# Kernel tuning notes

Measured on AMD Instinct MI355X. Metric: run time of the kernel, lower is better.

Reference implementation:

```python
import jax, jax.numpy as jnp
import numpy as np

CLASS_NUM = 31
KERNEL_NUM = 5
KERNEL_MUL = 2.0


def setup_inputs() -> dict:
    key = jax.random.key(0)
    k1, k2, k3, k4 = jax.random.split(key, 4)
    B, D = 4096, 256
    source = jax.random.normal(k1, (B, D), dtype=jnp.float32)
    target = jax.random.normal(k2, (B, D), dtype=jnp.float32)
    s_label = jax.random.randint(k3, (B,), 0, CLASS_NUM, dtype=jnp.int64)
    t_label = jax.random.uniform(k4, (B, CLASS_NUM), dtype=jnp.float32)
    return {"source": source, "target": target, "s_label": s_label, "t_label": t_label}


def _cal_weight(s_label, t_label):
    # Source: one-hot, column-normalized (empty classes -> divide by 100)
    s_onehot = jax.nn.one_hot(s_label, CLASS_NUM, dtype=jnp.float32)
    s_cnt = jnp.sum(s_onehot, axis=0)
    s_vec = s_onehot / jnp.where(s_cnt == 0, 100.0, s_cnt)
    # Target: soft probs, column-normalized (detached in original)
    t_prob = jax.lax.stop_gradient(t_label)
    t_cnt = jnp.sum(t_prob, axis=0)
    t_vec = t_prob / jnp.where(t_cnt == 0, 100.0, t_cnt)
    # Classes present in BOTH source labels and target argmax predictions
    t_arg = jnp.argmax(t_prob, axis=1)
    t_present = jnp.sum(jax.nn.one_hot(t_arg, CLASS_NUM, dtype=jnp.float32), axis=0) > 0
    mask = ((s_cnt > 0) & t_present).astype(jnp.float32)
    n_idx = jnp.maximum(jnp.sum(mask), 1.0)
    s_vec = s_vec * mask
    t_vec = t_vec * mask
    w_ss = (s_vec @ s_vec.T) / n_idx
    w_tt = (t_vec @ t_vec.T) / n_idx
    w_st = (s_vec @ t_vec.T) / n_idx
    return w_ss, w_tt, w_st


def reference(source, target, s_label, t_label):
    B = source.shape[0]
    w_ss, w_tt, w_st = _cal_weight(s_label, t_label)

    # Multi-bandwidth RBF kernel over concatenated samples
    total = jnp.concatenate([source, target], axis=0)  # [2B, D]
    sq = jnp.sum(total * total, axis=1)
    l2 = jnp.maximum(sq[:, None] + sq[None, :] - 2.0 * (total @ total.T), 0.0)  # [2B, 2B]

    n = 2 * B
    bw = jnp.sum(jax.lax.stop_gradient(l2)) / float(max(n * n - n, 1))
    bw = jnp.maximum(bw, 1e-6) / (KERNEL_MUL ** (KERNEL_NUM // 2))
    kernels = jnp.zeros_like(l2)
    for i in range(KERNEL_NUM):
        kernels = kernels + jnp.exp(-l2 / jnp.maximum(bw * KERNEL_MUL ** i, 1e-6))

    ss = kernels[:B, :B]
    tt = kernels[B:, B:]
    st = kernels[:B, B:]
    loss = jnp.sum(w_ss * ss + w_tt * tt - 2.0 * w_st * st)
    return loss
```

## Files before the change

### kernel.cpp

```cpp
#include <hip/hip_runtime.h>


#define B 4096
#define D 256
#define C 31
#define N2 8192
#define NTILE 64
#define NBLK (NTILE * (NTILE + 1) / 2)

typedef __attribute__((ext_vector_type(8))) short bf16x8;
typedef __attribute__((ext_vector_type(4))) float f32x4;

struct WS {
  double sum_sq;
  double Msum[256];
  int s_cnt[32];
  float t_cnt[32];
  int t_pres[32];
  float s_div[32], t_div[32];
  float inv_n_idx;
  float inv_d4;
  float sq[N2];
  int slab[N2];
  float sdv[N2];
  alignas(16) unsigned char Thi8[(size_t)N2 * D];
  alignas(16) unsigned short vhi[(size_t)N2 * 32];
  alignas(16) float v[(size_t)N2 * 32];
  alignas(16) double part[NBLK];
};

static __device__ __forceinline__ unsigned short f2bf(float f) {
  unsigned int u = __float_as_uint(f);
  return (unsigned short)((u + 0x7fffu + ((u >> 16) & 1u)) >> 16);
}
static __device__ __forceinline__ float bf2f(unsigned short s) {
  return __uint_as_float(((unsigned int)s) << 16);
}

#define GLD16(gsrc, ldst)                                                     \
  __builtin_amdgcn_global_load_lds(                                           \
      (const __attribute__((address_space(1))) void*)(gsrc),                  \
      (__attribute__((address_space(3))) void*)(ldst), 16, 0, 0)

__global__ void k0_init(WS* __restrict__ ws) {
  int tid = threadIdx.x;
  if (tid == 0) ws->sum_sq = 0.0;
  if (tid < 32) {
    ws->s_cnt[tid] = 0;
    ws->t_cnt[tid] = 0.f;
    ws->t_pres[tid] = 0;
  }
  ws->Msum[tid] = 0.0;
}

__global__ void kA1_stats(const int* __restrict__ s_label,
                          const float* __restrict__ t_label,
                          WS* __restrict__ ws) {
  __shared__ int ls[32];
  __shared__ float lt[32];
  __shared__ int lpres[32];
  int tid = threadIdx.x, lane = tid & 63;
  if (tid < 32) { ls[tid] = 0; lt[tid] = 0.f; lpres[tid] = 0; }
  __syncthreads();
  int row = blockIdx.x * 256 + tid;
  atomicAdd(&ls[s_label[row]], 1);
  const float* r = t_label + (size_t)row * C;
  float best = -1e30f;
  int barg = 0;
#pragma unroll
  for (int c = 0; c < C; ++c) {
    float x = r[c];
    if (x > best) { best = x; barg = c; }
    float s = x;
#pragma unroll
    for (int off = 32; off; off >>= 1) s += __shfl_down(s, off, 64);
    if (lane == 0) atomicAdd(&lt[c], s);
  }
  lpres[barg] = 1;
  __syncthreads();
  if (tid < 32) {
    if (ls[tid]) atomicAdd(&ws->s_cnt[tid], ls[tid]);
    atomicAdd(&ws->t_cnt[tid], lt[tid]);
    if (lpres[tid]) ws->t_pres[tid] = 1;
  }
}

__global__ void kA2_final(WS* __restrict__ ws) {
  int tid = threadIdx.x;
  int m = 0;
  if (tid < 32) {
    int cnt = ws->s_cnt[tid];
    m = (tid < C) && (cnt > 0) && (ws->t_pres[tid] != 0);
    ws->s_div[tid] = m ? 1.f / (float)cnt : 0.f;
    float t = ws->t_cnt[tid];
    float ta = (t == 0.f) ? 100.f : t;
    ws->t_div[tid] = m ? 1.f / ta : 0.f;
  }
  unsigned long long bal = __ballot(m);
  if (tid == 0) ws->inv_n_idx = 1.f / fmaxf((float)__popcll(bal), 1.f);
}

__global__ __launch_bounds__(256) void kB_prep(const float* __restrict__ src,
                                               const float* __restrict__ tgt,
                                               const int* __restrict__ s_label,
                                               const float* __restrict__ t_label,
                                               WS* __restrict__ ws) {
  int tid = threadIdx.x, w = tid >> 6, lane = tid & 63;
  int r0 = blockIdx.x * 32;
  __shared__ float rsq[32];
  __shared__ float colp[4][256];
  float ca0 = 0.f, ca1 = 0.f, ca2 = 0.f, ca3 = 0.f;
  int sc = lane >> 4, gl = (lane >> 1) & 7, hf = lane & 1;
#pragma unroll
  for (int i = 0; i < 8; ++i) {
    int rr = w * 8 + i;
    int p = r0 + rr;
    const float* rp = (p < B) ? src + (size_t)p * D : tgt + (size_t)(p - B) * D;
    float4 x = *(const float4*)(rp + lane * 4);
    unsigned int pk = __builtin_amdgcn_cvt_pk_fp8_f32(x.x, x.y, 0, false);
    pk = __builtin_amdgcn_cvt_pk_fp8_f32(x.z, x.w, pk, true);
    int gp = (gl + p + (p >> 1)) & 7;
    *(unsigned int*)(&ws->Thi8[(size_t)p * D + sc * 64 + gp * 8 + hf * 4]) = pk;
    ca0 += x.x; ca1 += x.y; ca2 += x.z; ca3 += x.w;
    float s = x.x * x.x + x.y * x.y + x.z * x.z + x.w * x.w;
#pragma unroll
    for (int off = 32; off; off >>= 1) s += __shfl_down(s, off, 64);
    if (lane == 0) rsq[rr] = s;
  }
  colp[w][lane * 4 + 0] = ca0;
  colp[w][lane * 4 + 1] = ca1;
  colp[w][lane * 4 + 2] = ca2;
  colp[w][lane * 4 + 3] = ca3;
  __syncthreads();
  if (tid < 32) {
    int p = r0 + tid;
    ws->sq[p] = rsq[tid];
    if (p < B) {
      int lb = s_label[p];
      ws->slab[p] = lb;
      ws->sdv[p] = ws->s_div[lb];
    } else {
      ws->slab[p] = 0;
      ws->sdv[p] = 0.f;
    }
  }
  if (tid < 64) {
    float ss = (tid < 32) ? rsq[tid] : 0.f;
#pragma unroll
    for (int off = 32; off; off >>= 1) ss += __shfl_down(ss, off, 64);
    if (tid == 0) atomicAdd(&ws->sum_sq, (double)ss);
  }
  atomicAdd(&ws->Msum[tid],
            (double)(colp[0][tid] + colp[1][tid] + colp[2][tid] + colp[3][tid]));
  int vr = tid >> 3, cb = (tid & 7) * 4;
  int p = r0 + vr;
  float vals[4];
#pragma unroll
  for (int j = 0; j < 4; ++j) {
    int c = cb + j;
    float val = 0.f;
    if (c < C) {
      if (p < B)
        val = (s_label[p] == c) ? ws->s_div[c] : 0.f;
      else
        val = -t_label[(size_t)(p - B) * C + c] * ws->t_div[c];
    }
    vals[j] = val;
  }
  float4 vf; vf.x = vals[0]; vf.y = vals[1]; vf.z = vals[2]; vf.w = vals[3];
  *(float4*)(&ws->v[(size_t)p * 32 + cb]) = vf;
  ushort4 vh;
  vh.x = f2bf(vals[0]); vh.y = f2bf(vals[1]);
  vh.z = f2bf(vals[2]); vh.w = f2bf(vals[3]);
  *(ushort4*)(&ws->vhi[(size_t)p * 32 + cb]) = vh;
}

__global__ void kC_bw(WS* __restrict__ ws) {
  int lane = threadIdx.x;
  double msq = 0.0;
#pragma unroll
  for (int i = 0; i < 4; ++i) {
    double m = ws->Msum[i * 64 + lane];
    msq += m * m;
  }
#pragma unroll
  for (int off = 32; off; off >>= 1) msq += __shfl_down(msq, off, 64);
  if (lane == 0) {
    double S = ws->sum_sq;
    double n = (double)N2;
    double sum_l2 = 2.0 * n * S - 2.0 * msq;
    double bw = sum_l2 / (n * n - n);
    bw = fmax(bw, 1e-6) * 0.25;
    double dc4 = fmax(bw * 16.0, 1e-6);
    ws->inv_d4 = (float)(1.0 / dc4);
  }
}

template <int KIND, bool DIAG>
static __device__ __forceinline__ float epi_ss_st(
    const f32x4 (&acc)[4][4], const WS* __restrict__ ws,
    const unsigned short* Vsw, int p0, int q0, int wr, int wc, int mrow,
    int quad) {
  float cinv = ws->inv_d4;
  float k2 = 2.f * cinv;
  float cq[4], sdq[4];
  int lq[4];
#pragma unroll
  for (int tj = 0; tj < 4; ++tj) {
    int q = q0 + wc + tj * 16 + mrow;
    cq[tj] = -cinv * ws->sq[q];
    if (KIND == 0) {
      lq[tj] = ws->slab[q];
      sdq[tj] = ws->sdv[q];
    }
  }
  float local = 0.f;
#pragma unroll
  for (int ti = 0; ti < 4; ++ti) {
#pragma unroll
    for (int rg = 0; rg < 4; ++rg) {
      int p = p0 + wr + ti * 16 + quad * 4 + rg;
      float cpl = -cinv * ws->sq[p];
      int lp = ws->slab[p];
      float sp = ws->sdv[p];
#pragma unroll
      for (int tj = 0; tj < 4; ++tj) {
        float z = fminf(fmaf(k2, acc[ti][tj][rg], cpl + cq[tj]), 0.f);
        float y = __expf(z);
        float kv = y;
        y *= y; kv += y;
        y *= y; kv += y;
        y *= y; kv += y;
        y *= y; kv += y;
        float wv;
        if (KIND == 0) {
          wv = (lp == lq[tj]) ? sp * sdq[tj] : 0.f;
        } else {
          int ql = wc + tj * 16 + mrow;
          wv = sp * bf2f(Vsw[ql * 32 + ((lp + ql) & 31)]);
        }
        if (DIAG) {
          int q = q0 + wc + tj * 16 + mrow;
          float f = (q > p) ? 2.f : ((q == p) ? 1.f : 0.f);
          local = fmaf(wv * f, kv, local);
        } else {
          local = fmaf(wv, kv, local);
        }
      }
    }
  }
  if (!DIAG) local *= 2.f;
  return local;
}

template <bool DIAG>
static __device__ __forceinline__ float epi_tt(const f32x4 (&acc)[4][4],
                                               const WS* __restrict__ ws,
                                               const unsigned short* SA,
                                               const unsigned short* SB,
                                               int p0, int q0, int wr, int wc,
                                               int mrow, int quad) {
  float cinv = ws->inv_d4;
  float k2 = 2.f * cinv;
  float cq[4];
#pragma unroll
  for (int tj = 0; tj < 4; ++tj)
    cq[tj] = -cinv * ws->sq[q0 + wc + tj * 16 + mrow];
  float cp[16];
#pragma unroll
  for (int ti = 0; ti < 4; ++ti)
#pragma unroll
    for (int rg = 0; rg < 4; ++rg)
      cp[ti * 4 + rg] = -cinv * ws->sq[p0 + wr + ti * 16 + quad * 4 + rg];
  bf16x8 af[4], bfr[4];
#pragma unroll
  for (int ti = 0; ti < 4; ++ti)
    af[ti] = *(const bf16x8*)(SA + (wr + ti * 16 + mrow) * 32 + quad * 8);
#pragma unroll
  for (int tj = 0; tj < 4; ++tj)
    bfr[tj] = *(const bf16x8*)(SB + (wc + tj * 16 + mrow) * 32 + quad * 8);
  float local = 0.f;
#pragma unroll
  for (int ti = 0; ti < 4; ++ti) {
#pragma unroll
    for (int tj = 0; tj < 4; ++tj) {
      f32x4 wv4 = __builtin_amdgcn_mfma_f32_16x16x32_bf16(
          af[ti], bfr[tj], (f32x4){0.f, 0.f, 0.f, 0.f}, 0, 0, 0);
#pragma unroll
      for (int rg = 0; rg < 4; ++rg) {
        float z = fminf(fmaf(k2, acc[ti][tj][rg], cp[ti * 4 + rg] + cq[tj]), 0.f);
        float y = __expf(z);
        float kv = y;
        y *= y; kv += y;
        y *= y; kv += y;
        y *= y; kv += y;
        y *= y; kv += y;
        if (DIAG) {
          int p = p0 + wr + ti * 16 + quad * 4 + rg;
          int q = q0 + wc + tj * 16 + mrow;
          float f = (q > p) ? 2.f : ((q == p) ? 1.f : 0.f);
          local = fmaf(wv4[rg] * f, kv, local);
        } else {
          local = fmaf(wv4[rg], kv, local);
        }
      }
    }
  }
  if (!DIAG) local *= 2.f;
  return local;
}

__global__ __launch_bounds__(256, 3) void k3_main(WS* __restrict__ ws) {
  int tid = threadIdx.x, w = tid >> 6, lane = tid & 63;
  int lin0 = blockIdx.x;
  int e = (lin0 & 7) * (NBLK / 8) + (lin0 >> 3);
  int b = 0, nb = 484, rem = e;
  while (rem >= nb) { rem -= nb; ++b; nb -= 64; }
  int base = b * 8;
  int bq_, r;
  if (rem < 36) {
    bq_ = 0;
    while ((bq_ + 1) * (bq_ + 2) / 2 <= rem) ++bq_;
    r = rem - (bq_ * (bq_ + 1)) / 2;
  } else {
    int t = rem - 36;
    bq_ = 8 + (t >> 3);
    r = t & 7;
  }
  int bp = base + r, bq = base + bq_;
  int p0 = bp * 128, q0 = bq * 128;

  bool is_ss = (bq < 32);
  bool is_tt = (bp >= 32);

  __shared__ __align__(16) unsigned char S[2][2][8192];
  unsigned short* Vsw = (unsigned short*)&S[0][0][0];
  unsigned short* SA = (unsigned short*)&S[0][0][0];
  unsigned short* SB = (unsigned short*)&S[0][1][0];
  double* red = (double*)&S[1][0][0];

  const int wr = (w >> 1) * 64, wc = (w & 1) * 64;
  const int mrow = lane & 15, quad = lane >> 4;
  f32x4 acc[4][4];
#pragma unroll
  for (int i = 0; i < 4; ++i)
#pragma unroll
    for (int j = 0; j < 4; ++j) acc[i][j] = (f32x4){0.f, 0.f, 0.f, 0.f};

  const unsigned char* T8 = ws->Thi8;
  int rA = tid >> 2, cb16 = (tid & 3) * 16, cp8 = (tid & 3) * 8;
  const unsigned char* a_lo = T8 + (size_t)(p0 + rA) * D + cb16;
  const unsigned char* a_hi = a_lo + (size_t)64 * D;
  const unsigned char* b_lo = T8 + (size_t)(q0 + rA) * D + cb16;
  const unsigned char* b_hi = b_lo + (size_t)64 * D;

#define STAGE(bufi, off)                                                      \
  do {                                                                        \
    GLD16(a_lo + (off), &S[bufi][0][w * 1024]);                               \
    GLD16(a_hi + (off), &S[bufi][0][w * 1024 + 4096]);                        \
    GLD16(b_lo + (off), &S[bufi][1][w * 1024]);                               \
    GLD16(b_hi + (off), &S[bufi][1][w * 1024 + 4096]);                        \
  } while (0)

  int aAdr[4], bAdr[4];
#pragma unroll
  for (int ti = 0; ti < 4; ++ti) {
    int Ra = wr + ti * 16 + mrow;
    aAdr[ti] = Ra * 64 + (((quad + Ra + (Ra >> 1)) & 7) << 3);
    int Rb = wc + ti * 16 + mrow;
    bAdr[ti] = Rb * 64 + (((quad + Rb + (Rb >> 1)) & 7) << 3);
  }

  STAGE(0, 0);
  __syncthreads();

#pragma unroll
  for (int i = 0; i < 4; ++i) {
    const int bufi = i & 1;
    if (i < 3) STAGE(bufi ^ 1, (i + 1) * 64);
    if (i == 3 && is_tt) {
      const unsigned short* gA = ws->vhi + (size_t)(p0 + rA) * 32 + cp8;
      const unsigned short* gB = ws->vhi + (size_t)(q0 + rA) * 32 + cp8;
      GLD16(gA, &S[0][0][w * 1024]);
      GLD16(gA + (size_t)64 * 32, &S[0][0][w * 1024 + 4096]);
      GLD16(gB, &S[0][1][w * 1024]);
      GLD16(gB + (size_t)64 * 32, &S[0][1][w * 1024 + 4096]);
    }
    const unsigned char* fb = &S[bufi][0][0];
#pragma unroll
    for (int t = 0; t < 2; ++t) {
      const int x = t << 5;
      long aF[4], bF[4];
#pragma unroll
      for (int ti = 0; ti < 4; ++ti)
        aF[ti] = *(const long*)(fb + (aAdr[ti] ^ x));
#pragma unroll
      for (int tj = 0; tj < 4; ++tj)
        bF[tj] = *(const long*)(fb + 8192 + (bAdr[tj] ^ x));
#pragma unroll
      for (int ti = 0; ti < 4; ++ti)
#pragma unroll
        for (int tj = 0; tj < 4; ++tj)
          acc[ti][tj] = __builtin_amdgcn_mfma_f32_16x16x32_fp8_fp8(
              aF[ti], bF[tj], acc[ti][tj], 0, 0, 0);
    }
    if (i < 3) __syncthreads();
  }

  if (!is_ss && !is_tt) {
    int rr = tid >> 1, h = (tid & 1) * 16;
    const float* vrow = ws->v + (size_t)(q0 + rr) * 32 + h;
#pragma unroll
    for (int j = 0; j < 16; ++j)
      Vsw[rr * 32 + ((h + j + rr) & 31)] = f2bf(vrow[j]);
  }
  __syncthreads();

  float local;
  if (is_ss) {
    if (bp == bq)
      local = epi_ss_st<0, true>(acc, ws, Vsw, p0, q0, wr, wc, mrow, quad);
    else
      local = epi_ss_st<0, false>(acc, ws, Vsw, p0, q0, wr, wc, mrow, quad);
  } else if (!is_tt) {
    local = epi_ss_st<1, false>(acc, ws, Vsw, p0, q0, wr, wc, mrow, quad);
  } else {
    if (bp == bq)
      local = epi_tt<true>(acc, ws, SA, SB, p0, q0, wr, wc, mrow, quad);
    else
      local = epi_tt<false>(acc, ws, SA, SB, p0, q0, wr, wc, mrow, quad);
  }

  double dl = (double)local;
#pragma unroll
  for (int off = 32; off; off >>= 1) dl += __shfl_down(dl, off, 64);
  if (lane == 0) red[w] = dl;
  __syncthreads();
  if (tid == 0) ws->part[lin0] = red[0] + red[1] + red[2] + red[3];
#undef STAGE
}

__global__ __launch_bounds__(256) void k4_out(WS* __restrict__ ws,
                                              float* __restrict__ out) {
  __shared__ double sh[4];
  int tid = threadIdx.x, w = tid >> 6, lane = tid & 63;
  double s = 0.0;
  for (int i = tid; i < NBLK; i += 256) s += ws->part[i];
#pragma unroll
  for (int off = 32; off; off >>= 1) s += __shfl_down(s, off, 64);
  if (lane == 0) sh[w] = s;
  __syncthreads();
  if (tid == 0)
    out[0] = (float)((sh[0] + sh[1] + sh[2] + sh[3]) * (double)ws->inv_n_idx);
}

extern "C" void kernel_launch(void* const* d_in, const int* in_sizes, int n_in,
                              void* d_out, int out_size, void* d_ws, size_t ws_size,
                              hipStream_t stream) {
  const float* src = (const float*)d_in[0];
  const float* tgt = (const float*)d_in[1];
  const int* s_label = (const int*)d_in[2];
  const float* t_label = (const float*)d_in[3];
  float* out = (float*)d_out;
  WS* ws = (WS*)d_ws;

  k0_init<<<1, 256, 0, stream>>>(ws);
  kA1_stats<<<16, 256, 0, stream>>>(s_label, t_label, ws);
  kA2_final<<<1, 64, 0, stream>>>(ws);
  kB_prep<<<256, 256, 0, stream>>>(src, tgt, s_label, t_label, ws);
  kC_bw<<<1, 64, 0, stream>>>(ws);
  k3_main<<<NBLK, 256, 0, stream>>>(ws);
  k4_out<<<1, 256, 0, stream>>>(ws, out);
}
```

Baseline: 132.5 us.

## Fuse prep stages into fewer launches and stage per-tile row data in LDS

Folds the label statistics into the feature prep kernel, and merges the bandwidth computation, weight finalisation and v-vector build into one kernel. This cuts the pre-pass from four launches to two. The main kernel now loads each tile's squared norms, labels and per-row divisors into LDS once, and prefetches the bf16 v rows during the MMA loop instead of converting fp32 rows after it. In exchange the per-class stats use more shared atomics per row, and the v build becomes a separate 32-block pass.

```diff
diff --git a/kernel.cpp b/kernel.cpp
--- a/kernel.cpp
+++ b/kernel.cpp
@@ -1,4 +1,5 @@
 #include <hip/hip_runtime.h>
+#include <cstddef>
 
 
 #define B 4096
@@ -17,7 +18,6 @@
   int s_cnt[32];
   float t_cnt[32];
   int t_pres[32];
-  float s_div[32], t_div[32];
   float inv_n_idx;
   float inv_d4;
   float sq[N2];
@@ -53,62 +53,19 @@
   ws->Msum[tid] = 0.0;
 }
 
-__global__ void kA1_stats(const int* __restrict__ s_label,
-                          const float* __restrict__ t_label,
-                          WS* __restrict__ ws) {
-  __shared__ int ls[32];
-  __shared__ float lt[32];
-  __shared__ int lpres[32];
-  int tid = threadIdx.x, lane = tid & 63;
-  if (tid < 32) { ls[tid] = 0; lt[tid] = 0.f; lpres[tid] = 0; }
-  __syncthreads();
-  int row = blockIdx.x * 256 + tid;
-  atomicAdd(&ls[s_label[row]], 1);
-  const float* r = t_label + (size_t)row * C;
-  float best = -1e30f;
-  int barg = 0;
-#pragma unroll
-  for (int c = 0; c < C; ++c) {
-    float x = r[c];
-    if (x > best) { best = x; barg = c; }
-    float s = x;
-#pragma unroll
-    for (int off = 32; off; off >>= 1) s += __shfl_down(s, off, 64);
-    if (lane == 0) atomicAdd(&lt[c], s);
-  }
-  lpres[barg] = 1;
-  __syncthreads();
-  if (tid < 32) {
-    if (ls[tid]) atomicAdd(&ws->s_cnt[tid], ls[tid]);
-    atomicAdd(&ws->t_cnt[tid], lt[tid]);
-    if (lpres[tid]) ws->t_pres[tid] = 1;
-  }
-}
-
-__global__ void kA2_final(WS* __restrict__ ws) {
-  int tid = threadIdx.x;
-  int m = 0;
-  if (tid < 32) {
-    int cnt = ws->s_cnt[tid];
-    m = (tid < C) && (cnt > 0) && (ws->t_pres[tid] != 0);
-    ws->s_div[tid] = m ? 1.f / (float)cnt : 0.f;
-    float t = ws->t_cnt[tid];
-    float ta = (t == 0.f) ? 100.f : t;
-    ws->t_div[tid] = m ? 1.f / ta : 0.f;
-  }
-  unsigned long long bal = __ballot(m);
-  if (tid == 0) ws->inv_n_idx = 1.f / fmaxf((float)__popcll(bal), 1.f);
-}
-
-__global__ __launch_bounds__(256) void kB_prep(const float* __restrict__ src,
-                                               const float* __restrict__ tgt,
-                                               const int* __restrict__ s_label,
-                                               const float* __restrict__ t_label,
-                                               WS* __restrict__ ws) {
+__global__ __launch_bounds__(256) void kPrep(const float* __restrict__ src,
+                                             const float* __restrict__ tgt,
+                                             const int* __restrict__ s_label,
+                                             const float* __restrict__ t_label,
+                                             WS* __restrict__ ws) {
   int tid = threadIdx.x, w = tid >> 6, lane = tid & 63;
   int r0 = blockIdx.x * 32;
   __shared__ float rsq[32];
   __shared__ float colp[4][256];
+  __shared__ int ls[32];
+  __shared__ float lt[32];
+  __shared__ int lpres[32];
+  if (tid < 32) { ls[tid] = 0; lt[tid] = 0.f; lpres[tid] = 0; }
   float ca0 = 0.f, ca1 = 0.f, ca2 = 0.f, ca3 = 0.f;
   int sc = lane >> 4, gl = (lane >> 1) & 7, hf = lane & 1;
 #pragma unroll
@@ -138,10 +95,19 @@
     if (p < B) {
       int lb = s_label[p];
       ws->slab[p] = lb;
-      ws->sdv[p] = ws->s_div[lb];
+      atomicAdd(&ls[lb], 1);
     } else {
       ws->slab[p] = 0;
-      ws->sdv[p] = 0.f;
+      const float* r = t_label + (size_t)(p - B) * C;
+      float best = -1e30f;
+      int barg = 0;
+#pragma unroll
+      for (int c = 0; c < C; ++c) {
+        float x = r[c];
+        if (x > best) { best = x; barg = c; }
+        atomicAdd(&lt[c], x);
+      }
+      lpres[barg] = 1;
     }
   }
   if (tid < 64) {
@@ -152,66 +118,95 @@
   }
   atomicAdd(&ws->Msum[tid],
             (double)(colp[0][tid] + colp[1][tid] + colp[2][tid] + colp[3][tid]));
-  int vr = tid >> 3, cb = (tid & 7) * 4;
-  int p = r0 + vr;
-  float vals[4];
-#pragma unroll
-  for (int j = 0; j < 4; ++j) {
-    int c = cb + j;
-    float val = 0.f;
-    if (c < C) {
-      if (p < B)
-        val = (s_label[p] == c) ? ws->s_div[c] : 0.f;
-      else
-        val = -t_label[(size_t)(p - B) * C + c] * ws->t_div[c];
-    }
-    vals[j] = val;
-  }
-  float4 vf; vf.x = vals[0]; vf.y = vals[1]; vf.z = vals[2]; vf.w = vals[3];
-  *(float4*)(&ws->v[(size_t)p * 32 + cb]) = vf;
-  ushort4 vh;
-  vh.x = f2bf(vals[0]); vh.y = f2bf(vals[1]);
-  vh.z = f2bf(vals[2]); vh.w = f2bf(vals[3]);
-  *(ushort4*)(&ws->vhi[(size_t)p * 32 + cb]) = vh;
-}
-
-__global__ void kC_bw(WS* __restrict__ ws) {
-  int lane = threadIdx.x;
-  double msq = 0.0;
-#pragma unroll
-  for (int i = 0; i < 4; ++i) {
-    double m = ws->Msum[i * 64 + lane];
-    msq += m * m;
-  }
-#pragma unroll
-  for (int off = 32; off; off >>= 1) msq += __shfl_down(msq, off, 64);
-  if (lane == 0) {
-    double S = ws->sum_sq;
-    double n = (double)N2;
-    double sum_l2 = 2.0 * n * S - 2.0 * msq;
-    double bw = sum_l2 / (n * n - n);
-    bw = fmax(bw, 1e-6) * 0.25;
-    double dc4 = fmax(bw * 16.0, 1e-6);
-    ws->inv_d4 = (float)(1.0 / dc4);
+  __syncthreads();
+  if (tid < 32) {
+    if (r0 < B) {
+      if (ls[tid]) atomicAdd(&ws->s_cnt[tid], ls[tid]);
+    } else {
+      atomicAdd(&ws->t_cnt[tid], lt[tid]);
+      if (lpres[tid]) ws->t_pres[tid] = 1;
+    }
+  }
+}
+
+__global__ __launch_bounds__(256) void kFin(const int* __restrict__ s_label,
+                                            const float* __restrict__ t_label,
+                                            WS* __restrict__ ws) {
+  int tid = threadIdx.x;
+  __shared__ float sdiv[32], tdiv[32];
+  if (tid < 64) {
+    int m = 0;
+    if (tid < 32) {
+      int cnt = ws->s_cnt[tid];
+      m = (tid < C) && (cnt > 0) && (ws->t_pres[tid] != 0);
+      sdiv[tid] = m ? 1.f / (float)cnt : 0.f;
+      float t = ws->t_cnt[tid];
+      tdiv[tid] = m ? 1.f / ((t == 0.f) ? 100.f : t) : 0.f;
+    }
+    unsigned long long bal = __ballot(m);
+    if (tid == 0 && blockIdx.x == 0)
+      ws->inv_n_idx = 1.f / fmaxf((float)__popcll(bal), 1.f);
+  } else if (tid < 128 && blockIdx.x == 0) {
+    int lane = tid - 64;
+    double msq = 0.0;
+#pragma unroll
+    for (int i = 0; i < 4; ++i) {
+      double mm = ws->Msum[i * 64 + lane];
+      msq += mm * mm;
+    }
+#pragma unroll
+    for (int off = 32; off; off >>= 1) msq += __shfl_down(msq, off, 64);
+    if (lane == 0) {
+      double S = ws->sum_sq;
+      double n = (double)N2;
+      double sum_l2 = 2.0 * n * S - 2.0 * msq;
+      double bw = sum_l2 / (n * n - n);
+      bw = fmax(bw, 1e-6) * 0.25;
+      ws->inv_d4 = (float)(1.0 / fmax(bw * 16.0, 1e-6));
+    }
+  }
+  __syncthreads();
+  int p = blockIdx.x * 256 + tid;
+  float vrow[32];
+  if (p < B) {
+    int lb = s_label[p];
+    float sv = sdiv[lb];
+    ws->sdv[p] = sv;
+#pragma unroll
+    for (int c = 0; c < 32; ++c) vrow[c] = (c == lb) ? sv : 0.f;
+  } else {
+    ws->sdv[p] = 0.f;
+    const float* r = t_label + (size_t)(p - B) * C;
+#pragma unroll
+    for (int c = 0; c < 32; ++c) vrow[c] = (c < C) ? -r[c] * tdiv[c] : 0.f;
+  }
+#pragma unroll
+  for (int k = 0; k < 8; ++k) {
+    float4 vf;
+    vf.x = vrow[k * 4 + 0]; vf.y = vrow[k * 4 + 1];
+    vf.z = vrow[k * 4 + 2]; vf.w = vrow[k * 4 + 3];
+    *(float4*)(&ws->v[(size_t)p * 32 + k * 4]) = vf;
+    ushort4 vh;
+    vh.x = f2bf(vf.x); vh.y = f2bf(vf.y); vh.z = f2bf(vf.z); vh.w = f2bf(vf.w);
+    *(ushort4*)(&ws->vhi[(size_t)p * 32 + k * 4]) = vh;
   }
 }
 
 template <int KIND, bool DIAG>
 static __device__ __forceinline__ float epi_ss_st(
-    const f32x4 (&acc)[4][4], const WS* __restrict__ ws,
-    const unsigned short* Vsw, int p0, int q0, int wr, int wc, int mrow,
-    int quad) {
-  float cinv = ws->inv_d4;
+    const f32x4 (&acc)[4][4], float cinv, const float* tSq, const int* tSlab,
+    const float* tSdv, const unsigned short* Vsw, int p0, int q0, int wr,
+    int wc, int mrow, int quad) {
   float k2 = 2.f * cinv;
   float cq[4], sdq[4];
   int lq[4];
 #pragma unroll
   for (int tj = 0; tj < 4; ++tj) {
-    int q = q0 + wc + tj * 16 + mrow;
-    cq[tj] = -cinv * ws->sq[q];
+    int iq = 128 + wc + tj * 16 + mrow;
+    cq[tj] = -cinv * tSq[iq];
     if (KIND == 0) {
-      lq[tj] = ws->slab[q];
-      sdq[tj] = ws->sdv[q];
+      lq[tj] = tSlab[iq];
+      sdq[tj] = tSdv[iq];
     }
   }
   float local = 0.f;
@@ -219,10 +214,10 @@
   for (int ti = 0; ti < 4; ++ti) {
 #pragma unroll
     for (int rg = 0; rg < 4; ++rg) {
-      int p = p0 + wr + ti * 16 + quad * 4 + rg;
-      float cpl = -cinv * ws->sq[p];
-      int lp = ws->slab[p];
-      float sp = ws->sdv[p];
+      int ip = wr + ti * 16 + quad * 4 + rg;
+      float cpl = -cinv * tSq[ip];
+      int lp = tSlab[ip];
+      float sp = tSdv[ip];
 #pragma unroll
       for (int tj = 0; tj < 4; ++tj) {
         float z = fminf(fmaf(k2, acc[ti][tj][rg], cpl + cq[tj]), 0.f);
@@ -240,6 +235,7 @@
           wv = sp * bf2f(Vsw[ql * 32 + ((lp + ql) & 31)]);
         }
         if (DIAG) {
+          int p = p0 + ip;
           int q = q0 + wc + tj * 16 + mrow;
           float f = (q > p) ? 2.f : ((q == p) ? 1.f : 0.f);
           local = fmaf(wv * f, kv, local);
@@ -255,23 +251,22 @@
 
 template <bool DIAG>
 static __device__ __forceinline__ float epi_tt(const f32x4 (&acc)[4][4],
-                                               const WS* __restrict__ ws,
+                                               float cinv, const float* tSq,
                                                const unsigned short* SA,
                                                const unsigned short* SB,
                                                int p0, int q0, int wr, int wc,
                                                int mrow, int quad) {
-  float cinv = ws->inv_d4;
   float k2 = 2.f * cinv;
   float cq[4];
 #pragma unroll
   for (int tj = 0; tj < 4; ++tj)
-    cq[tj] = -cinv * ws->sq[q0 + wc + tj * 16 + mrow];
+    cq[tj] = -cinv * tSq[128 + wc + tj * 16 + mrow];
   float cp[16];
 #pragma unroll
   for (int ti = 0; ti < 4; ++ti)
 #pragma unroll
     for (int rg = 0; rg < 4; ++rg)
-      cp[ti * 4 + rg] = -cinv * ws->sq[p0 + wr + ti * 16 + quad * 4 + rg];
+      cp[ti * 4 + rg] = -cinv * tSq[wr + ti * 16 + quad * 4 + rg];
   bf16x8 af[4], bfr[4];
 #pragma unroll
   for (int ti = 0; ti < 4; ++ti)
@@ -332,8 +327,12 @@
 
   bool is_ss = (bq < 32);
   bool is_tt = (bp >= 32);
+  bool is_st = !is_ss && !is_tt;
 
   __shared__ __align__(16) unsigned char S[2][2][8192];
+  __shared__ __align__(16) float tSq[256];
+  __shared__ __align__(16) int tSlab[256];
+  __shared__ __align__(16) float tSdv[256];
   unsigned short* Vsw = (unsigned short*)&S[0][0][0];
   unsigned short* SA = (unsigned short*)&S[0][0][0];
   unsigned short* SB = (unsigned short*)&S[0][1][0];
@@ -371,6 +370,8 @@
     bAdr[ti] = Rb * 64 + (((quad + Rb + (Rb >> 1)) & 7) << 3);
   }
 
+  uint4 stv0 = {0, 0, 0, 0}, stv1 = {0, 0, 0, 0};
+
   STAGE(0, 0);
   __syncthreads();
 
@@ -378,6 +379,22 @@
   for (int i = 0; i < 4; ++i) {
     const int bufi = i & 1;
     if (i < 3) STAGE(bufi ^ 1, (i + 1) * 64);
+    if (i == 0 && w == 0) {
+      int l32 = lane & 31;
+      const float* s1 = ((lane < 32) ? ws->sq + p0 : ws->sq + q0) + l32 * 4;
+      GLD16(s1, tSq);
+      const int* s2 = ((lane < 32) ? ws->slab + p0 : ws->slab + q0) + l32 * 4;
+      GLD16(s2, tSlab);
+      const float* s3 = ((lane < 32) ? ws->sdv + p0 : ws->sdv + q0) + l32 * 4;
+      GLD16(s3, tSdv);
+    }
+    if (i == 2 && is_st) {
+      const uint4* vsrc = (const uint4*)(ws->vhi +
+                                         (size_t)(q0 + (tid >> 1)) * 32 +
+                                         (tid & 1) * 16);
+      stv0 = vsrc[0];
+      stv1 = vsrc[1];
+    }
     if (i == 3 && is_tt) {
       const unsigned short* gA = ws->vhi + (size_t)(p0 + rA) * 32 + cp8;
       const unsigned short* gB = ws->vhi + (size_t)(q0 + rA) * 32 + cp8;
@@ -407,28 +424,35 @@
     if (i < 3) __syncthreads();
   }
 
-  if (!is_ss && !is_tt) {
+  if (is_st) {
     int rr = tid >> 1, h = (tid & 1) * 16;
-    const float* vrow = ws->v + (size_t)(q0 + rr) * 32 + h;
-#pragma unroll
-    for (int j = 0; j < 16; ++j)
-      Vsw[rr * 32 + ((h + j + rr) & 31)] = f2bf(vrow[j]);
-  }
-  __syncthreads();
-
+    unsigned int uu[8] = {stv0.x, stv0.y, stv0.z, stv0.w,
+                          stv1.x, stv1.y, stv1.z, stv1.w};
+#pragma unroll
+    for (int j = 0; j < 8; ++j) {
+      Vsw[rr * 32 + ((h + 2 * j + rr) & 31)] = (unsigned short)(uu[j] & 0xffff);
+      Vsw[rr * 32 + ((h + 2 * j + 1 + rr) & 31)] = (unsigned short)(uu[j] >> 16);
+    }
+  }
+  __syncthreads();
+
+  float cinv = ws->inv_d4;
   float local;
   if (is_ss) {
     if (bp == bq)
-      local = epi_ss_st<0, true>(acc, ws, Vsw, p0, q0, wr, wc, mrow, quad);
+      local = epi_ss_st<0, true>(acc, cinv, tSq, tSlab, tSdv, Vsw, p0, q0, wr,
+                                 wc, mrow, quad);
     else
-      local = epi_ss_st<0, false>(acc, ws, Vsw, p0, q0, wr, wc, mrow, quad);
-  } else if (!is_tt) {
-    local = epi_ss_st<1, false>(acc, ws, Vsw, p0, q0, wr, wc, mrow, quad);
+      local = epi_ss_st<0, false>(acc, cinv, tSq, tSlab, tSdv, Vsw, p0, q0, wr,
+                                  wc, mrow, quad);
+  } else if (is_st) {
+    local = epi_ss_st<1, false>(acc, cinv, tSq, tSlab, tSdv, Vsw, p0, q0, wr,
+                                wc, mrow, quad);
   } else {
     if (bp == bq)
-      local = epi_tt<true>(acc, ws, SA, SB, p0, q0, wr, wc, mrow, quad);
+      local = epi_tt<true>(acc, cinv, tSq, SA, SB, p0, q0, wr, wc, mrow, quad);
     else
-      local = epi_tt<false>(acc, ws, SA, SB, p0, q0, wr, wc, mrow, quad);
+      local = epi_tt<false>(acc, cinv, tSq, SA, SB, p0, q0, wr, wc, mrow, quad);
   }
 
   double dl = (double)local;
@@ -465,10 +489,8 @@
   WS* ws = (WS*)d_ws;
 
   k0_init<<<1, 256, 0, stream>>>(ws);
-  kA1_stats<<<16, 256, 0, stream>>>(s_label, t_label, ws);
-  kA2_final<<<1, 64, 0, stream>>>(ws);
-  kB_prep<<<256, 256, 0, stream>>>(src, tgt, s_label, t_label, ws);
-  kC_bw<<<1, 64, 0, stream>>>(ws);
+  kPrep<<<256, 256, 0, stream>>>(src, tgt, s_label, t_label, ws);
+  kFin<<<32, 256, 0, stream>>>(s_label, t_label, ws);
   k3_main<<<NBLK, 256, 0, stream>>>(ws);
   k4_out<<<1, 256, 0, stream>>>(ws, out);
 }
```

After: 150.1 us. 1.13x slower.
